# Performance work log

Measured on AMD Instinct MI355X. Metric: run time of the kernel, lower is better.

The kernel has to match this reference:

```python
import jax, jax.numpy as jnp
import numpy as np

B, T, I, H, NL, HORIZON, NQ = 256, 512, 64, 512, 2, 30, 3
MEDIAN_IDX = 1  # quantiles.index(0.5)


def _lstm_cell(xt, h, c, Wih, Whh, b):
    # PyTorch gate order: i, f, g, o
    g = xt @ Wih.T + h @ Whh.T + b
    i, f, gg, o = jnp.split(g, 4, axis=-1)
    c_new = jax.nn.sigmoid(f) * c + jax.nn.sigmoid(i) * jnp.tanh(gg)
    h_new = jax.nn.sigmoid(o) * jnp.tanh(c_new)
    return h_new, c_new


def _run_lstm_layer(xs, Wih, Whh, b):
    # xs: [T, B, in]; zero initial state (torch default)
    batch = xs.shape[1]
    hidden = Whh.shape[1]
    h0 = jnp.zeros((batch, hidden), xs.dtype)

    def step(carry, xt):
        h, c = carry
        h, c = _lstm_cell(xt, h, c, Wih, Whh, b)
        return (h, c), h

    (hT, cT), hs = jax.lax.scan(step, (h0, h0), xs)
    return hs, hT, cT


def setup_inputs() -> dict:
    key = jax.random.key(0)
    ks = jax.random.split(key, 24)
    k = 1.0 / np.sqrt(H)

    def u(kk, shape):
        return jax.random.uniform(kk, shape, jnp.float32, -k, k)

    inp = {
        "x": jax.random.normal(ks[0], (B, T, I), jnp.float32),
        # encoder layer 0 (input I) and layer 1 (input H)
        "enc_Wih0": u(ks[1], (4 * H, I)),
        "enc_Whh0": u(ks[2], (4 * H, H)),
        "enc_bih0": u(ks[3], (4 * H,)),
        "enc_bhh0": u(ks[4], (4 * H,)),
        "enc_Wih1": u(ks[5], (4 * H, H)),
        "enc_Whh1": u(ks[6], (4 * H, H)),
        "enc_bih1": u(ks[7], (4 * H,)),
        "enc_bhh1": u(ks[8], (4 * H,)),
        # decoder layer 0 (input H+1) and layer 1 (input H)
        "dec_Wih0": u(ks[9], (4 * H, H + 1)),
        "dec_Whh0": u(ks[10], (4 * H, H)),
        "dec_bih0": u(ks[11], (4 * H,)),
        "dec_bhh0": u(ks[12], (4 * H,)),
        "dec_Wih1": u(ks[13], (4 * H, H)),
        "dec_Whh1": u(ks[14], (4 * H, H)),
        "dec_bih1": u(ks[15], (4 * H,)),
        "dec_bhh1": u(ks[16], (4 * H,)),
        # attention: W [H,H] (no bias), V [H] (Linear(H,1) weight)
        "attn_W": u(ks[17], (H, H)),
        "attn_v": u(ks[18], (H,)),
        # output projection [NQ, H] + bias
        "out_W": u(ks[19], (NQ, H)),
        "out_b": u(ks[20], (NQ,)),
    }
    return inp


def reference(x, enc_Wih0, enc_Whh0, enc_bih0, enc_bhh0,
              enc_Wih1, enc_Whh1, enc_bih1, enc_bhh1,
              dec_Wih0, dec_Whh0, dec_bih0, dec_bhh0,
              dec_Wih1, dec_Whh1, dec_bih1, dec_bhh1,
              attn_W, attn_v, out_W, out_b):
    # ---- encoder: 2-layer LSTM over time (eval mode: no dropout) ----
    xs = jnp.transpose(x, (1, 0, 2))  # [T, B, I]
    hs0, _, _ = _run_lstm_layer(xs, enc_Wih0, enc_Whh0, enc_bih0 + enc_bhh0)
    hs1, h_last, c_last = _run_lstm_layer(hs0, enc_Wih1, enc_Whh1, enc_bih1 + enc_bhh1)
    encoder_outputs = jnp.transpose(hs1, (1, 0, 2))  # [B, T, H]

    # precompute W(encoder_outputs) once (same math as per-step recompute)
    enc_proj = jnp.einsum('bth,gh->btg', encoder_outputs, attn_W)  # [B, T, H]

    b_dec0 = dec_bih0 + dec_bhh0
    b_dec1 = dec_bih1 + dec_bhh1

    dec_input0 = x[:, -1, 0:1]  # [B, 1]

    def step(carry, _):
        h, c, inp = carry
        # Bahdanau attention
        dec_proj = h @ attn_W.T  # [B, H]
        energies = jnp.einsum('bth,h->bt', jnp.tanh(enc_proj + dec_proj[:, None, :]), attn_v)
        attn = jax.nn.softmax(energies, axis=1)  # [B, T]
        ctx = jnp.einsum('bt,bth->bh', attn, encoder_outputs)  # [B, H]
        # decoder LSTM, 1 timestep; both layers restart from the SAME (h, c)
        # (the module repeats the last layer's state across layers each step)
        x0 = jnp.concatenate([inp, ctx], axis=1)  # [B, H+1]
        h0, c0 = _lstm_cell(x0, h, c, dec_Wih0, dec_Whh0, b_dec0)
        h1, c1 = _lstm_cell(h0, h, c, dec_Wih1, dec_Whh1, b_dec1)
        out = h1 @ out_W.T + out_b  # [B, NQ]
        new_inp = out[:, MEDIAN_IDX:MEDIAN_IDX + 1]  # feed back median quantile
        return (h1, c1, new_inp), out

    _, preds = jax.lax.scan(step, (h_last, c_last, dec_input0), None, length=HORIZON)
    return jnp.transpose(preds, (1, 0, 2))  # [B, HORIZON, NQ]
```

## Files before the change

kernel.cpp:

```cpp
#include <hip/hip_runtime.h>


typedef _Float16 half_t;
typedef __attribute__((ext_vector_type(8)))  _Float16 f16x8;
typedef __attribute__((ext_vector_type(16))) float    f32x16;

#define MFMA(a,b,c) __builtin_amdgcn_mfma_f32_32x32x16_f16((a),(b),(c),0,0,0)
#define CBAR()      asm volatile("" ::: "memory")
#define AUXC 17

template<int N> __device__ __forceinline__ void waitvm() {
  asm volatile("s_waitcnt vmcnt(%0)" :: "n"(N) : "memory");
}

__device__ __forceinline__ float fsig(float x)  { return 1.0f / (1.0f + __expf(-x)); }
__device__ __forceinline__ float ftanh(float x) { return 1.0f - 2.0f / (1.0f + __expf(2.0f * x)); }

union FU { float f; unsigned u; };
union HU { _Float16 h; unsigned short u; };
__device__ __forceinline__ float ldfa(const float* p) {
  unsigned v = __hip_atomic_load((const unsigned*)p, __ATOMIC_RELAXED, __HIP_MEMORY_SCOPE_AGENT);
  FU c; c.u = v; return c.f;
}
__device__ __forceinline__ void stfa(float* p, float v) {
  FU c; c.f = v;
  __hip_atomic_store((unsigned*)p, c.u, __ATOMIC_RELAXED, __HIP_MEMORY_SCOPE_AGENT);
}
__device__ __forceinline__ void stha(half_t* p, float v) {
  HU c; c.h = (half_t)v;
  __hip_atomic_store((unsigned short*)p, c.u, __ATOMIC_RELAXED, __HIP_MEMORY_SCOPE_AGENT);
}
__device__ __forceinline__ void st64(float* p, float a, float b) {
  FU x, y; x.f = a; y.f = b;
  unsigned long long v = (unsigned long long)x.u | ((unsigned long long)y.u << 32);
  __hip_atomic_store((unsigned long long*)p, v, __ATOMIC_RELAXED, __HIP_MEMORY_SCOPE_AGENT);
}
__device__ __forceinline__ void ld64(const float* p, float& a, float& b) {
  unsigned long long v = __hip_atomic_load((const unsigned long long*)p, __ATOMIC_RELAXED, __HIP_MEMORY_SCOPE_AGENT);
  FU x, y; x.u = (unsigned)v; y.u = (unsigned)(v >> 32); a = x.f; b = y.f;
}

static constexpr size_t O_X16 = 0;
static constexpr size_t O_WL0 = O_X16 + (size_t)512*256*128*2;
static constexpr size_t O_WL1 = O_WL0 + (size_t)2048*640*2;
static constexpr size_t O_WP1 = O_WL1 + (size_t)2048*1024*2;
static constexpr size_t O_WD0 = O_WP1 + (size_t)4672*512*2;
static constexpr size_t O_WD1 = O_WD0 + (size_t)2048*512*2;
static constexpr size_t O_BL0 = O_WD1 + (size_t)2048*512*2;
static constexpr size_t O_BL1 = O_BL0 + 8192;
static constexpr size_t O_BD0 = O_BL1 + 8192;
static constexpr size_t O_BD1 = O_BD0 + 8192;
static constexpr size_t O_W0C = O_BD1 + 8192;
static constexpr size_t O_H0B = O_W0C + 8192;
static constexpr size_t O_H1B = O_H0B + (size_t)2*256*512*2;
static constexpr size_t O_HD1 = O_H1B + (size_t)2*256*512*2;
static constexpr size_t O_H0D = O_HD1 + (size_t)256*512*2;
static constexpr size_t O_CTX = O_H0D + (size_t)256*512*2;
static constexpr size_t O_C0  = O_CTX + (size_t)256*512*2;
static constexpr size_t O_C1  = O_C0  + (size_t)256*512*4;
static constexpr size_t O_INP = O_C1  + (size_t)256*512*4;
static constexpr size_t O_GAT = O_INP + 1024;
static constexpr size_t O_EO  = O_GAT + (size_t)256*4672*4;
static constexpr size_t O_EP  = O_EO  + (size_t)256*512*512*2;
static constexpr size_t WS_NEED = O_EP + (size_t)256*512*512*2;

__device__ __align__(4096) unsigned char g_ws[WS_NEED];
__device__ int g_bar[2048];
__device__ int g_flags[1024];

#define WSH(o) ((half_t*)(g_ws + (o)))
#define WSCH(o) ((const half_t*)(g_ws + (o)))
#define WSF(o) ((float*)(g_ws + (o)))
#define WSCF(o) ((const float*)(g_ws + (o)))
#define BLINE(i) (g_bar + ((size_t)(i) << 5))

__device__ __forceinline__ int gperm(int n) { return (n & 3) * 512 + (n >> 2); }

__device__ __forceinline__ void gbarf(int g, int r, int step) {
  __syncthreads();
  if (threadIdx.x < 64) {
    if (threadIdx.x == 0)
      __hip_atomic_store(&g_flags[(g << 6) + r], step,
                         __ATOMIC_RELAXED, __HIP_MEMORY_SCOPE_AGENT);
    const int* fp = &g_flags[(g << 6) + threadIdx.x];
    for (;;) {
      int v = __hip_atomic_load(fp, __ATOMIC_RELAXED, __HIP_MEMORY_SCOPE_AGENT);
      if (__all(v >= step)) break;
      __builtin_amdgcn_s_sleep(1);
    }
  }
  __syncthreads();
}

__device__ __forceinline__ void gbar_acq(int g, int sub) {
  __syncthreads();
  if (threadIdx.x == 0) {
    int* cnt = BLINE(g * 2 + sub);
    int* mst = BLINE(8 + g);
    int* gs  = BLINE(12 + g * 2 + sub);
    int old = __hip_atomic_load(gs, __ATOMIC_RELAXED, __HIP_MEMORY_SCOPE_AGENT);
    int a = __hip_atomic_fetch_add(cnt, 1, __ATOMIC_ACQ_REL, __HIP_MEMORY_SCOPE_AGENT);
    if (a == 31) {
      __hip_atomic_store(cnt, 0, __ATOMIC_RELAXED, __HIP_MEMORY_SCOPE_AGENT);
      int m = __hip_atomic_fetch_add(mst, 1, __ATOMIC_ACQ_REL, __HIP_MEMORY_SCOPE_AGENT);
      if (m == 1) {
        __hip_atomic_store(mst, 0, __ATOMIC_RELAXED, __HIP_MEMORY_SCOPE_AGENT);
        __hip_atomic_fetch_add(BLINE(12 + g * 2), 1, __ATOMIC_RELEASE, __HIP_MEMORY_SCOPE_AGENT);
        __hip_atomic_fetch_add(BLINE(12 + g * 2 + 1), 1, __ATOMIC_RELEASE, __HIP_MEMORY_SCOPE_AGENT);
      }
    }
    while (__hip_atomic_load(gs, __ATOMIC_RELAXED, __HIP_MEMORY_SCOPE_AGENT) == old)
      __builtin_amdgcn_s_sleep(2);
    (void)__hip_atomic_load(gs, __ATOMIC_ACQUIRE, __HIP_MEMORY_SCOPE_AGENT);
  }
  __syncthreads();
}

struct Seg { const half_t* p; int stride; int row0; };

template<int AXA, int AXB>
__device__ __forceinline__ void stageA(Seg sa, Seg sb, int cSplit, int c,
                                       int lane, int wid, char* dst) {
  bool isA = c < cSplit;
  Seg s = isA ? sa : sb;
  int kb = (isA ? c : (c - cSplit)) * 128;
  const half_t* g = s.p + (size_t)(s.row0 + (lane & 31)) * s.stride
                        + kb + (wid << 4) + ((lane >> 5) << 3);
  if (isA) {
    __builtin_amdgcn_global_load_lds(
        (const __attribute__((address_space(1))) unsigned int*)g,
        (__attribute__((address_space(3))) unsigned int*)dst, 16, 0, AXA);
    __builtin_amdgcn_global_load_lds(
        (const __attribute__((address_space(1))) unsigned int*)(g + (size_t)32 * s.stride),
        (__attribute__((address_space(3))) unsigned int*)(dst + 1024), 16, 0, AXA);
  } else {
    __builtin_amdgcn_global_load_lds(
        (const __attribute__((address_space(1))) unsigned int*)g,
        (__attribute__((address_space(3))) unsigned int*)dst, 16, 0, AXB);
    __builtin_amdgcn_global_load_lds(
        (const __attribute__((address_space(1))) unsigned int*)(g + (size_t)32 * s.stride),
        (__attribute__((address_space(3))) unsigned int*)(dst + 1024), 16, 0, AXB);
  }
}

template<int C, int NC, int CSPLIT, int AXA, int AXB>
__device__ __forceinline__ void kreg(Seg sa, Seg sb,
                                     const f16x8 (&B0)[8], const f16x8 (&B1)[8],
                                     int lane, int wid, char* asg, f32x16 acc[2][2]) {
  if constexpr (C < NC) {
    constexpr int rem = NC - 1 - C;
    waitvm<2 * (rem < 3 ? rem : 3)>();
    char* ab = asg + (size_t)(((C & 3) * 8 + wid)) * 2048 + lane * 16;
    f16x8 a0 = *(const f16x8*)ab;
    f16x8 a1 = *(const f16x8*)(ab + 1024);
    acc[0][0] = MFMA(a0, B0[C], acc[0][0]);
    acc[0][1] = MFMA(a0, B1[C], acc[0][1]);
    acc[1][0] = MFMA(a1, B0[C], acc[1][0]);
    acc[1][1] = MFMA(a1, B1[C], acc[1][1]);
    if constexpr (C + 4 < NC)
      stageA<AXA, AXB>(sa, sb, CSPLIT, C + 4, lane, wid,
                       asg + (size_t)((((C + 4) & 3) * 8 + wid)) * 2048);
    CBAR();
    kreg<C + 1, NC, CSPLIT, AXA, AXB>(sa, sb, B0, B1, lane, wid, asg, acc);
  }
}

template<int NC, int CSPLIT, int AXA, int AXB>
__device__ __forceinline__ void gemm_regB(Seg sa, Seg sb,
                                          const f16x8 (&B0)[8], const f16x8 (&B1)[8],
                                          int lane, int wid, char* asg, f32x16 acc[2][2]) {
  #pragma unroll
  for (int c = 0; c < (NC < 4 ? NC : 4); c++) {
    stageA<AXA, AXB>(sa, sb, CSPLIT, c, lane, wid, asg + (size_t)((c & 3) * 8 + wid) * 2048);
    CBAR();
  }
  kreg<0, NC, CSPLIT, AXA, AXB>(sa, sb, B0, B1, lane, wid, asg, acc);
}

template<int C, int NC>
__device__ __forceinline__ void kks(int lane, int wid, char* asg, f32x16 acc[2][2],
                                    f16x8 (&b0)[4], f16x8 (&b1)[4]) {
  if constexpr (C < NC) {
    waitvm<4 * (NC - 1 - C)>();
    char* ab = asg + (size_t)(C * 8 + wid) * 2048 + lane * 16;
    f16x8 a0 = *(const f16x8*)ab;
    f16x8 a1 = *(const f16x8*)(ab + 1024);
    acc[0][0] = MFMA(a0, b0[C], acc[0][0]);
    acc[0][1] = MFMA(a0, b1[C], acc[0][1]);
    acc[1][0] = MFMA(a1, b0[C], acc[1][0]);
    acc[1][1] = MFMA(a1, b1[C], acc[1][1]);
    CBAR();
    kks<C + 1, NC>(lane, wid, asg, acc, b0, b1);
  }
}

template<int NC, int AXA, int AXB>
__device__ __forceinline__ void gemm_ks(Seg sa, Seg sb, int cSplit, const half_t* Wt,
                                        int lane, int wid, char* asg, f32x16 acc[2][2]) {
  const half_t* wb = Wt + (wid << 1) * 512 + lane * 8;
  f16x8 b0[4], b1[4];
  #pragma unroll
  for (int c = 0; c < NC; c++) {
    stageA<AXA, AXB>(sa, sb, cSplit, c, lane, wid, asg + (size_t)(c * 8 + wid) * 2048);
    CBAR();
    b0[c] = *(const f16x8*)(wb + (size_t)c * 8192);
    b1[c] = *(const f16x8*)(wb + (size_t)c * 8192 + 512);
    CBAR();
  }
  kks<0, NC>(lane, wid, asg, acc, b0, b1);
}

__device__ __forceinline__ void acc_wr(float* dst, int lane, f32x16 acc[2][2]) {
  #pragma unroll
  for (int t = 0; t < 4; t++) {
    f32x16 a = acc[t >> 1][t & 1];
    #pragma unroll
    for (int r4 = 0; r4 < 4; r4++)
      *(float4*)(dst + ((t * 4 + r4) * 64 + lane) * 4) =
          make_float4(a[r4*4], a[r4*4+1], a[r4*4+2], a[r4*4+3]);
  }
}
__device__ __forceinline__ void acc_add(const float* src, int lane, f32x16 acc[2][2]) {
  #pragma unroll
  for (int t = 0; t < 4; t++) {
    #pragma unroll
    for (int r4 = 0; r4 < 4; r4++) {
      float4 v = *(const float4*)(src + ((t * 4 + r4) * 64 + lane) * 4);
      acc[t>>1][t&1][r4*4]   += v.x;
      acc[t>>1][t&1][r4*4+1] += v.y;
      acc[t>>1][t&1][r4*4+2] += v.z;
      acc[t>>1][t&1][r4*4+3] += v.w;
    }
  }
}
__device__ __forceinline__ void reduce8(f32x16 acc[2][2], float* red, int lane, int wid) {
  if (wid >= 4) acc_wr(red + (size_t)(wid - 4) * 4096, lane, acc);
  __syncthreads();
  if (wid < 4) acc_add(red + (size_t)wid * 4096, lane, acc);
  if (wid == 2 || wid == 3) acc_wr(red + (size_t)wid * 4096, lane, acc);
  __syncthreads();
  if (wid < 2) {
    acc_add(red + (size_t)(wid + 2) * 4096, lane, acc);
    float* zone = red + 8192 + (size_t)wid * 4096;
    #pragma unroll
    for (int ms = 0; ms < 2; ms++)
      #pragma unroll
      for (int ns = 0; ns < 2; ns++)
        #pragma unroll
        for (int rr = 0; rr < 16; rr++) {
          int row = ms * 32 + (rr & 3) + ((rr >> 2) << 3) + ((lane >> 5) << 2);
          zone[row * 64 + ns * 32 + (lane & 31)] = acc[ms][ns][rr];
        }
  }
  __syncthreads();
}
__device__ __forceinline__ float4 rsum4(const float* red, int row, int col) {
  float4 a = *(const float4*)&red[8192 + row * 64 + col];
  float4 b = *(const float4*)&red[12288 + row * 64 + col];
  return make_float4(a.x + b.x, a.y + b.y, a.z + b.z, a.w + b.w);
}

__global__ void __launch_bounds__(512, 2) kmain(const float* __restrict__ attn_v,
                                                const float* __restrict__ out_b,
                                                float* __restrict__ out) {
  __shared__ __align__(16) char asg[65536];
  __shared__ float red[16384];

  const half_t* x16 = WSCH(O_X16);
  const half_t* wL0 = WSCH(O_WL0);
  const half_t* wL1 = WSCH(O_WL1);
  const half_t* wP1 = WSCH(O_WP1);
  const half_t* wD0 = WSCH(O_WD0);
  const half_t* wD1 = WSCH(O_WD1);
  half_t* h0bB = WSH(O_H0B);
  half_t* h1bB = WSH(O_H1B);
  half_t* hd1  = WSH(O_HD1);
  half_t* h0d  = WSH(O_H0D);
  half_t* ctx  = WSH(O_CTX);
  half_t* eo   = WSH(O_EO);
  half_t* ep   = WSH(O_EP);
  float* c1 = WSF(O_C1);
  float* inp = WSF(O_INP);
  float* gates = WSF(O_GAT);

  const int tid = threadIdx.x;
  const int wid = tid >> 6;
  const int lane = tid & 63;
  const int g = blockIdx.x & 3;
  const int r = blockIdx.x >> 2;
  const int sub = r & 1;
  const int m0 = g << 6;
  const f32x16 zv = {0,0,0,0,0,0,0,0,0,0,0,0,0,0,0,0};
  int bstep = 0;

  {
    const bool isL1 = r >= 32;
    const int n0 = (r & 31) << 6;

    const half_t* wbase = isL1 ? (wL1 + (size_t)(n0 >> 6) * (8 * 8192))
                               : (wL0 + (size_t)(n0 >> 6) * (5 * 8192));
    const half_t* wb = wbase + (wid << 1) * 512 + lane * 8;
    const int ncB = isL1 ? 8 : 5;
    f16x8 B0[8], B1[8];
    #pragma unroll
    for (int c = 0; c < 8; c++) {
      if (c < ncB) {
        B0[c] = *(const f16x8*)(wb + (size_t)c * 8192);
        B1[c] = *(const f16x8*)(wb + (size_t)c * 8192 + 512);
      }
    }
    const int eu = tid & 15;
    const int ebl = tid >> 4;
    const float* bias = isL1 ? WSCF(O_BL1) : WSCF(O_BL0);
    float4 breg = *(const float4*)&bias[n0 + eu * 4];
    float creg0 = 0.f, creg1 = 0.f;

    for (int s = 0; s <= 512; s++) {
      const bool active = isL1 ? (s > 0) : (s < 512);
      if (active) {
        const half_t* h0r = h0bB + (size_t)((s + 1) & 1) * (256 * 512);
        f32x16 acc[2][2] = {{zv, zv}, {zv, zv}};
        int t;
        if (!isL1) {
          t = s;
          gemm_regB<5, 1, 0, AUXC>(Seg{x16, 128, t * 256 + m0}, Seg{h0r, 512, m0},
                                   B0, B1, lane, wid, asg, acc);
        } else {
          t = s - 1;
          const half_t* h1r = h1bB + (size_t)(s & 1) * (256 * 512);
          gemm_regB<8, 4, AUXC, AUXC>(Seg{h0r, 512, m0}, Seg{h1r, 512, m0},
                                      B0, B1, lane, wid, asg, acc);
        }
        reduce8(acc, red, lane, wid);
        half_t* hb = isL1 ? (h1bB + (size_t)((s - 1) & 1) * (256 * 512))
                          : (h0bB + (size_t)(s & 1) * (256 * 512));
        #pragma unroll
        for (int it = 0; it < 2; it++) {
          int bl = ebl + it * 32;
          float4 g4 = rsum4(red, bl, eu * 4);
          float gi = g4.x + breg.x, gf = g4.y + breg.y;
          float gz = g4.z + breg.z, go = g4.w + breg.w;
          float cold = it ? creg1 : creg0;
          float cn = fsig(gf) * cold + fsig(gi) * ftanh(gz);
          float hn = fsig(go) * ftanh(cn);
          if (it) creg1 = cn; else creg0 = cn;
          int bg = m0 + bl, ug = (n0 >> 2) + eu;
          stha(&hb[bg * 512 + ug], hn);
          if (isL1) eo[((size_t)bg * 512 + t) * 512 + ug] = (half_t)hn;
        }
      }
      gbarf(g, r, ++bstep);
    }

    if (isL1) {
      int ug = (n0 >> 2) + eu;
      c1[(m0 + ebl) * 512 + ug] = creg0;
      c1[(m0 + ebl + 32) * 512 + ug] = creg1;
    }
  }
  gbar_acq(g, sub);

  for (int j = 0; j < 64; j++) {
    const int jj = r * 64 + j;
    const int ml = jj >> 3;
    const int nt = jj & 7;
    const int row0 = (g << 15) + ml * 64;
    f32x16 acc[2][2] = {{zv, zv}, {zv, zv}};
    gemm_ks<4, 0, 0>(Seg{eo, 512, row0}, Seg{eo, 512, row0}, 4,
                     wP1 + (size_t)nt * (4 * 8192), lane, wid, asg, acc);
    reduce8(acc, red, lane, wid);
    {
      int row = tid >> 3, col = (tid & 7) * 8;
      float4 a0 = rsum4(red, row, col);
      float4 a1 = rsum4(red, row, col + 4);
      f16x8 h8;
      h8[0] = (half_t)a0.x; h8[1] = (half_t)a0.y; h8[2] = (half_t)a0.z; h8[3] = (half_t)a0.w;
      h8[4] = (half_t)a1.x; h8[5] = (half_t)a1.y; h8[6] = (half_t)a1.z; h8[7] = (half_t)a1.w;
      *(f16x8*)&ep[(size_t)(row0 + row) * 512 + nt * 64 + col] = h8;
    }
    __syncthreads();
  }
  gbar_acq(g, sub);

  for (int d = 0; d <= 30; d++) {
    const half_t* hs = (d == 0) ? (h1bB + 256 * 512) : hd1;
    for (int jj = r; jj < 73; jj += 64) {
      const int n0p = jj * 64;
      f32x16 acc[2][2] = {{zv, zv}, {zv, zv}};
      gemm_ks<4, AUXC, AUXC>(Seg{hs, 512, m0}, Seg{hs, 512, m0}, 4,
                             wP1 + (size_t)jj * (4 * 8192), lane, wid, asg, acc);
      reduce8(acc, red, lane, wid);
      if (n0p < 4608) {
        #pragma unroll
        for (int it = 0; it < 2; it++) {
          int q = it * 512 + tid;
          int row = q >> 4, col = (q & 15) * 4;
          float4 v4 = rsum4(red, row, col);
          float* dst = &gates[(size_t)(m0 + row) * 4672 + n0p + col];
          st64(dst, v4.x, v4.y);
          st64(dst + 2, v4.z, v4.w);
        }
      } else if (d > 0) {
        if (tid < 64) {
          int bg = m0 + tid;
          float v0 = red[8192 + tid * 64 + 0] + red[12288 + tid * 64 + 0] + out_b[0];
          float v1 = red[8192 + tid * 64 + 1] + red[12288 + tid * 64 + 1] + out_b[1];
          float v2 = red[8192 + tid * 64 + 2] + red[12288 + tid * 64 + 2] + out_b[2];
          out[(size_t)bg * 90 + (d - 1) * 3 + 0] = v0;
          out[(size_t)bg * 90 + (d - 1) * 3 + 1] = v1;
          out[(size_t)bg * 90 + (d - 1) * 3 + 2] = v2;
          stfa(&inp[bg], v1);
        }
      }
      __syncthreads();
    }
    gbarf(g, r, ++bstep);
    if (d == 30) break;

    {
      const int b = m0 + r;
      float* dpb = red;
      float* vb  = red + 512;
      float* eb  = red + 1024;
      float* ab2 = red + 2048;
      float* sc  = red + 2560;
      float* pm  = red + 4096;
      dpb[tid] = ldfa(&gates[(size_t)b * 4672 + tid]);
      vb[tid]  = attn_v[tid];
      __syncthreads();
      float va[8], da[8];
      {
        float4 t0 = *(const float4*)&vb[lane * 8];
        float4 t1 = *(const float4*)&vb[lane * 8 + 4];
        float4 t2 = *(const float4*)&dpb[lane * 8];
        float4 t3 = *(const float4*)&dpb[lane * 8 + 4];
        va[0]=t0.x; va[1]=t0.y; va[2]=t0.z; va[3]=t0.w;
        va[4]=t1.x; va[5]=t1.y; va[6]=t1.z; va[7]=t1.w;
        da[0]=t2.x; da[1]=t2.y; da[2]=t2.z; da[3]=t2.w;
        da[4]=t3.x; da[5]=t3.y; da[6]=t3.z; da[7]=t3.w;
      }
      const half_t* eprow = ep + ((size_t)b << 18) + (size_t)(wid * 64) * 512 + lane * 8;
      for (int tt = 0; tt < 64; tt++) {
        f16x8 e8 = *(const f16x8*)(eprow + (size_t)tt * 512);
        float sum = 0.f;
        #pragma unroll
        for (int jq = 0; jq < 8; jq++)
          sum += va[jq] * ftanh((float)e8[jq] + da[jq]);
        #pragma unroll
        for (int off = 32; off > 0; off >>= 1) sum += __shfl_down(sum, off, 64);
        if (lane == 0) eb[wid * 64 + tt] = sum;
      }
      __syncthreads();
      float e0 = eb[tid];
      float mx = e0;
      #pragma unroll
      for (int off = 32; off > 0; off >>= 1) mx = fmaxf(mx, __shfl_xor(mx, off, 64));
      if (lane == 0) sc[wid] = mx;
      __syncthreads();
      mx = sc[0];
      #pragma unroll
      for (int q = 1; q < 8; q++) mx = fmaxf(mx, sc[q]);
      float x0 = __expf(e0 - mx);
      float ssum = x0;
      #pragma unroll
      for (int off = 32; off > 0; off >>= 1) ssum += __shfl_xor(ssum, off, 64);
      __syncthreads();
      if (lane == 0) sc[8 + wid] = ssum;
      __syncthreads();
      float tot = sc[8];
      #pragma unroll
      for (int q = 1; q < 8; q++) tot += sc[8 + q];
      float inv = 1.f / tot;
      ab2[tid] = x0 * inv;
      __syncthreads();
      float pacc[8] = {0,0,0,0,0,0,0,0};
      const half_t* eow = eo + ((size_t)b << 18) + (size_t)(wid * 64) * 512 + lane * 8;
      for (int tt = 0; tt < 64; tt++) {
        f16x8 h8 = *(const f16x8*)(eow + (size_t)tt * 512);
        float at = ab2[wid * 64 + tt];
        #pragma unroll
        for (int jq = 0; jq < 8; jq++) pacc[jq] += at * (float)h8[jq];
      }
      #pragma unroll
      for (int jq = 0; jq < 8; jq++) pm[wid * 512 + lane * 8 + jq] = pacc[jq];
      __syncthreads();
      float sctx = 0.f;
      #pragma unroll
      for (int w = 0; w < 8; w++) sctx += pm[w * 512 + tid];
      stha(&ctx[(b << 9) + tid], sctx);
    }
    gbarf(g, r, ++bstep);

    if (r < 32) {
      const int n0 = r << 6;
      f32x16 acc[2][2] = {{zv, zv}, {zv, zv}};
      gemm_ks<4, AUXC, AUXC>(Seg{ctx, 512, m0}, Seg{ctx, 512, m0}, 4,
                             wD0 + (size_t)(n0 >> 6) * (4 * 8192), lane, wid, asg, acc);
      reduce8(acc, red, lane, wid);
      const float* bD0 = WSCF(O_BD0);
      const float* w0c = WSCF(O_W0C);
      #pragma unroll
      for (int it = 0; it < 2; it++) {
        int q = it * 512 + tid;
        int u = q & 15, bl = q >> 4;
        int bg = m0 + bl, ug = (n0 >> 2) + u, nl = n0 + u * 4;
        float4 g4 = rsum4(red, bl, u * 4);
        float p0, p1, p2, p3;
        ld64(&gates[(size_t)bg * 4672 + 512 + nl], p0, p1);
        ld64(&gates[(size_t)bg * 4672 + 512 + nl + 2], p2, p3);
        float4 b4 = *(const float4*)&bD0[nl];
        float4 w4 = *(const float4*)&w0c[nl];
        float iv = ldfa(&inp[bg]);
        float gi = g4.x + p0 + b4.x + iv * w4.x;
        float gf = g4.y + p1 + b4.y + iv * w4.y;
        float gz = g4.z + p2 + b4.z + iv * w4.z;
        float go = g4.w + p3 + b4.w + iv * w4.w;
        float cold = c1[bg * 512 + ug];
        float cn = fsig(gf) * cold + fsig(gi) * ftanh(gz);
        stha(&h0d[bg * 512 + ug], fsig(go) * ftanh(cn));
      }
    }
    gbarf(g, r, ++bstep);

    if (r < 32) {
      const int n0 = r << 6;
      f32x16 acc[2][2] = {{zv, zv}, {zv, zv}};
      gemm_ks<4, AUXC, AUXC>(Seg{h0d, 512, m0}, Seg{h0d, 512, m0}, 4,
                             wD1 + (size_t)(n0 >> 6) * (4 * 8192), lane, wid, asg, acc);
      reduce8(acc, red, lane, wid);
      const float* bD1 = WSCF(O_BD1);
      #pragma unroll
      for (int it = 0; it < 2; it++) {
        int q = it * 512 + tid;
        int u = q & 15, bl = q >> 4;
        int bg = m0 + bl, ug = (n0 >> 2) + u, nl = n0 + u * 4;
        float4 g4 = rsum4(red, bl, u * 4);
        float p0, p1, p2, p3;
        ld64(&gates[(size_t)bg * 4672 + 2560 + nl], p0, p1);
        ld64(&gates[(size_t)bg * 4672 + 2560 + nl + 2], p2, p3);
        float4 b4 = *(const float4*)&bD1[nl];
        float gi = g4.x + p0 + b4.x;
        float gf = g4.y + p1 + b4.y;
        float gz = g4.z + p2 + b4.z;
        float go = g4.w + p3 + b4.w;
        float cold = c1[bg * 512 + ug];
        float cn = fsig(gf) * cold + fsig(gi) * ftanh(gz);
        float hn = fsig(go) * ftanh(cn);
        c1[bg * 512 + ug] = cn;
        stha(&hd1[bg * 512 + ug], hn);
      }
    }
    gbarf(g, r, ++bstep);
  }
}

__global__ void kpackB(size_t dstOff, int id, int Ntiles, int NC,
                       const float* s0, const float* s1,
                       const float* s2, const float* s3) {
  half_t* dst = (half_t*)(g_ws + dstOff);
  size_t total = (size_t)Ntiles * NC * 8192;
  size_t i = (size_t)blockIdx.x * 256 + threadIdx.x;
  size_t stride = (size_t)gridDim.x * 256;
  for (size_t e = i; e < total; e += stride) {
    int j = e & 7;
    int l = (e >> 3) & 63;
    int bh = (e >> 9) & 1;
    int w = (e >> 10) & 7;
    int tc = (int)(e >> 13);
    int c = tc % NC;
    int tile = tc / NC;
    int n = tile * 64 + bh * 32 + (l & 31);
    int k = c * 128 + w * 16 + ((l >> 5) << 3) + j;
    float v = 0.f;
    if (id == 0) {
      int pn = gperm(n);
      if (k < 64) v = s0[(size_t)pn * 64 + k];
      else if (k >= 128) v = s1[(size_t)pn * 512 + (k - 128)];
    } else if (id == 1) {
      int pn = gperm(n);
      v = (k < 512) ? s0[(size_t)pn * 512 + k] : s1[(size_t)pn * 512 + (k - 512)];
    } else if (id == 2) {
      if (n < 512) v = s0[((size_t)n << 9) + k];
      else if (n < 2560) v = s1[((size_t)gperm(n - 512) << 9) + k];
      else if (n < 4608) v = s2[((size_t)gperm(n - 2560) << 9) + k];
      else if (n < 4611) v = s3[((size_t)(n - 4608) << 9) + k];
    } else if (id == 3) {
      v = s0[(size_t)gperm(n) * 513 + 1 + k];
    } else {
      v = s0[((size_t)gperm(n) << 9) + k];
    }
    dst[e] = (half_t)v;
  }
}

__global__ void kmisc(const float* ebih0, const float* ebhh0, const float* ebih1, const float* ebhh1,
                      const float* dbih0, const float* dbhh0, const float* dbih1, const float* dbhh1,
                      const float* dWih0, const float* x) {
  float* bL0 = WSF(O_BL0);
  float* bL1 = WSF(O_BL1);
  float* bD0 = WSF(O_BD0);
  float* bD1 = WSF(O_BD1);
  float* w0c = WSF(O_W0C);
  half_t* h0b = WSH(O_H0B);
  half_t* h1b = WSH(O_H1B);
  float* c1 = WSF(O_C1);
  float* inp = WSF(O_INP);
  int i = blockIdx.x * 256 + threadIdx.x, stride = gridDim.x * 256;
  for (int idx = i; idx < 262144; idx += stride) {
    if (idx < 2048) {
      int pn = gperm(idx);
      bL0[idx] = ebih0[pn] + ebhh0[pn];
      bL1[idx] = ebih1[pn] + ebhh1[pn];
      bD0[idx] = dbih0[pn] + dbhh0[pn];
      bD1[idx] = dbih1[pn] + dbhh1[pn];
      w0c[idx] = dWih0[(size_t)pn * 513];
      g_bar[idx] = 0;
    }
    if (idx < 1024) g_flags[idx] = 0;
    if (idx < 256) inp[idx] = x[((size_t)idx * 512 + 511) * 64];
    h0b[idx] = (half_t)0.f;
    h1b[idx] = (half_t)0.f;
    if (idx < 131072) c1[idx] = 0.f;
  }
}

__global__ void kx16(const float* x) {
  half_t* dst = WSH(O_X16);
  size_t i = (size_t)blockIdx.x * 256 + threadIdx.x;
  size_t stride = (size_t)gridDim.x * 256;
  for (size_t e = i; e < (size_t)512 * 256 * 128; e += stride) {
    int t = (int)(e >> 15);
    int b = (int)((e >> 7) & 255);
    int ii = (int)(e & 127);
    dst[e] = (ii < 64) ? (half_t)x[((size_t)b * 512 + t) * 64 + ii] : (half_t)0.f;
  }
}

extern "C" void kernel_launch(void* const* d_in, const int* in_sizes, int n_in,
                              void* d_out, int out_size, void* d_ws, size_t ws_size,
                              hipStream_t stream) {
  const float* x     = (const float*)d_in[0];
  const float* eWih0 = (const float*)d_in[1];
  const float* eWhh0 = (const float*)d_in[2];
  const float* ebih0 = (const float*)d_in[3];
  const float* ebhh0 = (const float*)d_in[4];
  const float* eWih1 = (const float*)d_in[5];
  const float* eWhh1 = (const float*)d_in[6];
  const float* ebih1 = (const float*)d_in[7];
  const float* ebhh1 = (const float*)d_in[8];
  const float* dWih0 = (const float*)d_in[9];
  const float* dWhh0 = (const float*)d_in[10];
  const float* dbih0 = (const float*)d_in[11];
  const float* dbhh0 = (const float*)d_in[12];
  const float* dWih1 = (const float*)d_in[13];
  const float* dWhh1 = (const float*)d_in[14];
  const float* dbih1 = (const float*)d_in[15];
  const float* dbhh1 = (const float*)d_in[16];
  const float* attnW = (const float*)d_in[17];
  const float* attnv = (const float*)d_in[18];
  const float* outW  = (const float*)d_in[19];
  const float* outb  = (const float*)d_in[20];
  (void)in_sizes; (void)n_in; (void)out_size; (void)d_ws; (void)ws_size;

  kpackB<<<1024, 256, 0, stream>>>(O_WL0, 0, 32, 5, eWih0, eWhh0, nullptr, nullptr);
  kpackB<<<1024, 256, 0, stream>>>(O_WL1, 1, 32, 8, eWih1, eWhh1, nullptr, nullptr);
  kpackB<<<1024, 256, 0, stream>>>(O_WP1, 2, 73, 4, attnW, dWhh0, dWhh1, outW);
  kpackB<<<1024, 256, 0, stream>>>(O_WD0, 3, 32, 4, dWih0, nullptr, nullptr, nullptr);
  kpackB<<<1024, 256, 0, stream>>>(O_WD1, 4, 32, 4, dWih1, nullptr, nullptr, nullptr);
  kmisc<<<1024, 256, 0, stream>>>(ebih0, ebhh0, ebih1, ebhh1,
                                  dbih0, dbhh0, dbih1, dbhh1, dWih0, x);
  kx16<<<2048, 256, 0, stream>>>(x);

  float* outp = (float*)d_out;
  void* args[] = {(void*)&attnv, (void*)&outb, (void*)&outp};
  hipError_t e = hipLaunchCooperativeKernel((void*)kmain, dim3(256), dim3(512),
                                            args, 0, stream);
  if (e != hipSuccess) {
    kmain<<<dim3(256), dim3(512), 0, stream>>>(attnv, outb, outp);
  }
}
```

Before: 8.513 ms.

## Defer decoder layer-1 gate projections into idle phase and relax atomic loads

The decoder's per-step projection of 73 column tiles is split. Only 40 tiles plus the output tile are computed before the attention barrier, and the remaining 32 tiles (layer-1 input gates) are computed by the otherwise idle blocks during the decoder layer-0 phase, shortening the critical serial phase. Relaxed atomic loads become plain loads, with an acquire fence added after the spin barrier. The AUXC cache-policy bits on GEMM loads are set to zero. This risks memory-ordering subtleties, since correctness now relies on the fence and on cache behaviour rather than on per-load atomics.

```diff
diff --git a/kernel.cpp b/kernel.cpp
--- a/kernel.cpp
+++ b/kernel.cpp
@@ -7,7 +7,6 @@
 
 #define MFMA(a,b,c) __builtin_amdgcn_mfma_f32_32x32x16_f16((a),(b),(c),0,0,0)
 #define CBAR()      asm volatile("" ::: "memory")
-#define AUXC 17
 
 template<int N> __device__ __forceinline__ void waitvm() {
   asm volatile("s_waitcnt vmcnt(%0)" :: "n"(N) : "memory");
@@ -18,10 +17,7 @@
 
 union FU { float f; unsigned u; };
 union HU { _Float16 h; unsigned short u; };
-__device__ __forceinline__ float ldfa(const float* p) {
-  unsigned v = __hip_atomic_load((const unsigned*)p, __ATOMIC_RELAXED, __HIP_MEMORY_SCOPE_AGENT);
-  FU c; c.u = v; return c.f;
-}
+__device__ __forceinline__ float ldfa(const float* p) { return *p; }
 __device__ __forceinline__ void stfa(float* p, float v) {
   FU c; c.f = v;
   __hip_atomic_store((unsigned*)p, c.u, __ATOMIC_RELAXED, __HIP_MEMORY_SCOPE_AGENT);
@@ -36,8 +32,7 @@
   __hip_atomic_store((unsigned long long*)p, v, __ATOMIC_RELAXED, __HIP_MEMORY_SCOPE_AGENT);
 }
 __device__ __forceinline__ void ld64(const float* p, float& a, float& b) {
-  unsigned long long v = __hip_atomic_load((const unsigned long long*)p, __ATOMIC_RELAXED, __HIP_MEMORY_SCOPE_AGENT);
-  FU x, y; x.u = (unsigned)v; y.u = (unsigned)(v >> 32); a = x.f; b = y.f;
+  float2 v = *(const float2*)p; a = v.x; b = v.y;
 }
 
 static constexpr size_t O_X16 = 0;
@@ -88,6 +83,7 @@
       if (__all(v >= step)) break;
       __builtin_amdgcn_s_sleep(1);
     }
+    __builtin_amdgcn_fence(__ATOMIC_ACQUIRE, "agent");
   }
   __syncthreads();
 }
@@ -323,13 +319,13 @@
         int t;
         if (!isL1) {
           t = s;
-          gemm_regB<5, 1, 0, AUXC>(Seg{x16, 128, t * 256 + m0}, Seg{h0r, 512, m0},
-                                   B0, B1, lane, wid, asg, acc);
+          gemm_regB<5, 1, 0, 0>(Seg{x16, 128, t * 256 + m0}, Seg{h0r, 512, m0},
+                                B0, B1, lane, wid, asg, acc);
         } else {
           t = s - 1;
           const half_t* h1r = h1bB + (size_t)(s & 1) * (256 * 512);
-          gemm_regB<8, 4, AUXC, AUXC>(Seg{h0r, 512, m0}, Seg{h1r, 512, m0},
-                                      B0, B1, lane, wid, asg, acc);
+          gemm_regB<8, 4, 0, 0>(Seg{h0r, 512, m0}, Seg{h1r, 512, m0},
+                                B0, B1, lane, wid, asg, acc);
         }
         reduce8(acc, red, lane, wid);
         half_t* hb = isL1 ? (h1bB + (size_t)((s - 1) & 1) * (256 * 512))
@@ -384,35 +380,38 @@
 
   for (int d = 0; d <= 30; d++) {
     const half_t* hs = (d == 0) ? (h1bB + 256 * 512) : hd1;
-    for (int jj = r; jj < 73; jj += 64) {
-      const int n0p = jj * 64;
-      f32x16 acc[2][2] = {{zv, zv}, {zv, zv}};
-      gemm_ks<4, AUXC, AUXC>(Seg{hs, 512, m0}, Seg{hs, 512, m0}, 4,
-                             wP1 + (size_t)jj * (4 * 8192), lane, wid, asg, acc);
-      reduce8(acc, red, lane, wid);
-      if (n0p < 4608) {
-        #pragma unroll
-        for (int it = 0; it < 2; it++) {
-          int q = it * 512 + tid;
-          int row = q >> 4, col = (q & 15) * 4;
-          float4 v4 = rsum4(red, row, col);
-          float* dst = &gates[(size_t)(m0 + row) * 4672 + n0p + col];
-          st64(dst, v4.x, v4.y);
-          st64(dst + 2, v4.z, v4.w);
+
+    {
+      const int jj = (r < 40) ? r : ((r == 63) ? 72 : -1);
+      if (jj >= 0) {
+        const int n0p = jj * 64;
+        f32x16 acc[2][2] = {{zv, zv}, {zv, zv}};
+        gemm_ks<4, 0, 0>(Seg{hs, 512, m0}, Seg{hs, 512, m0}, 4,
+                         wP1 + (size_t)jj * (4 * 8192), lane, wid, asg, acc);
+        reduce8(acc, red, lane, wid);
+        if (n0p < 4608) {
+          #pragma unroll
+          for (int it = 0; it < 2; it++) {
+            int q = it * 512 + tid;
+            int row = q >> 4, col = (q & 15) * 4;
+            float4 v4 = rsum4(red, row, col);
+            float* dst = &gates[(size_t)(m0 + row) * 4672 + n0p + col];
+            st64(dst, v4.x, v4.y);
+            st64(dst + 2, v4.z, v4.w);
+          }
+        } else if (d > 0) {
+          if (tid < 64) {
+            int bg = m0 + tid;
+            float v0 = red[8192 + tid * 64 + 0] + red[12288 + tid * 64 + 0] + out_b[0];
+            float v1 = red[8192 + tid * 64 + 1] + red[12288 + tid * 64 + 1] + out_b[1];
+            float v2 = red[8192 + tid * 64 + 2] + red[12288 + tid * 64 + 2] + out_b[2];
+            out[(size_t)bg * 90 + (d - 1) * 3 + 0] = v0;
+            out[(size_t)bg * 90 + (d - 1) * 3 + 1] = v1;
+            out[(size_t)bg * 90 + (d - 1) * 3 + 2] = v2;
+            stfa(&inp[bg], v1);
+          }
         }
-      } else if (d > 0) {
-        if (tid < 64) {
-          int bg = m0 + tid;
-          float v0 = red[8192 + tid * 64 + 0] + red[12288 + tid * 64 + 0] + out_b[0];
-          float v1 = red[8192 + tid * 64 + 1] + red[12288 + tid * 64 + 1] + out_b[1];
-          float v2 = red[8192 + tid * 64 + 2] + red[12288 + tid * 64 + 2] + out_b[2];
-          out[(size_t)bg * 90 + (d - 1) * 3 + 0] = v0;
-          out[(size_t)bg * 90 + (d - 1) * 3 + 1] = v1;
-          out[(size_t)bg * 90 + (d - 1) * 3 + 2] = v2;
-          stfa(&inp[bg], v1);
-        }
-      }
-      __syncthreads();
+      }
     }
     gbarf(g, r, ++bstep);
     if (d == 30) break;
@@ -494,8 +493,8 @@
     if (r < 32) {
       const int n0 = r << 6;
       f32x16 acc[2][2] = {{zv, zv}, {zv, zv}};
-      gemm_ks<4, AUXC, AUXC>(Seg{ctx, 512, m0}, Seg{ctx, 512, m0}, 4,
-                             wD0 + (size_t)(n0 >> 6) * (4 * 8192), lane, wid, asg, acc);
+      gemm_ks<4, 0, 0>(Seg{ctx, 512, m0}, Seg{ctx, 512, m0}, 4,
+                       wD0 + (size_t)(n0 >> 6) * (4 * 8192), lane, wid, asg, acc);
       reduce8(acc, red, lane, wid);
       const float* bD0 = WSCF(O_BD0);
       const float* w0c = WSCF(O_W0C);
@@ -519,14 +518,30 @@
         float cn = fsig(gf) * cold + fsig(gi) * ftanh(gz);
         stha(&h0d[bg * 512 + ug], fsig(go) * ftanh(cn));
       }
+    } else {
+      const int jj = 8 + r;
+      const int n0p = jj * 64;
+      f32x16 acc[2][2] = {{zv, zv}, {zv, zv}};
+      gemm_ks<4, 0, 0>(Seg{hs, 512, m0}, Seg{hs, 512, m0}, 4,
+                       wP1 + (size_t)jj * (4 * 8192), lane, wid, asg, acc);
+      reduce8(acc, red, lane, wid);
+      #pragma unroll
+      for (int it = 0; it < 2; it++) {
+        int q = it * 512 + tid;
+        int row = q >> 4, col = (q & 15) * 4;
+        float4 v4 = rsum4(red, row, col);
+        float* dst = &gates[(size_t)(m0 + row) * 4672 + n0p + col];
+        st64(dst, v4.x, v4.y);
+        st64(dst + 2, v4.z, v4.w);
+      }
     }
     gbarf(g, r, ++bstep);
 
     if (r < 32) {
       const int n0 = r << 6;
       f32x16 acc[2][2] = {{zv, zv}, {zv, zv}};
-      gemm_ks<4, AUXC, AUXC>(Seg{h0d, 512, m0}, Seg{h0d, 512, m0}, 4,
-                             wD1 + (size_t)(n0 >> 6) * (4 * 8192), lane, wid, asg, acc);
+      gemm_ks<4, 0, 0>(Seg{h0d, 512, m0}, Seg{h0d, 512, m0}, 4,
+                       wD1 + (size_t)(n0 >> 6) * (4 * 8192), lane, wid, asg, acc);
       reduce8(acc, red, lane, wid);
       const float* bD1 = WSCF(O_BD1);
       #pragma unroll
```

After: 9.011 ms. +5.8%, slower.
